# Kernel optimization log

Hardware: AMD Instinct MI355X
Metric: run time of the kernel (lower is better)

## Reference

```python
import jax, jax.numpy as jnp
import numpy as np

N = 10000      # nodes
E = 320000     # edges (before self loops)
IN = 128       # in_channels
HID = 128      # hidden_channels
OUT = 64       # out_channels
H = 3          # heads
K = 10         # n_clusters
EDIM = 1       # edge_attr feature dim
NEG_SLOPE = 0.2


def setup_inputs() -> dict:
    key = jax.random.key(0)
    ks = jax.random.split(key, 24)
    x = jax.random.normal(ks[0], (N, IN), jnp.float32)
    src = jax.random.randint(ks[1], (E,), 0, N)
    dst = jax.random.randint(ks[2], (E,), 0, N)
    dst = jnp.where(src == dst, (dst + 1) % N, dst)  # avoid pre-existing self loops
    edge_index = jnp.stack([src, dst]).astype(jnp.int64)
    edge_attr = jax.random.uniform(ks[3], (E, EDIM), dtype=jnp.float32)
    s = 0.1
    inp = {
        'x': x, 'edge_index': edge_index, 'edge_attr': edge_attr,
        # GAT layer 1 params
        'W1': jax.random.normal(ks[4], (IN, H * HID), jnp.float32) * s,
        'att_s1': jax.random.normal(ks[5], (H, HID), jnp.float32) * s,
        'att_d1': jax.random.normal(ks[6], (H, HID), jnp.float32) * s,
        'We1': jax.random.normal(ks[7], (EDIM, H * HID), jnp.float32) * s,
        'att_e1': jax.random.normal(ks[8], (H, HID), jnp.float32) * s,
        'b1': jnp.zeros((H * HID,), jnp.float32),
        # GAT layer 2 params
        'W2': jax.random.normal(ks[9], (H * HID, H * OUT), jnp.float32) * s,
        'att_s2': jax.random.normal(ks[10], (H, OUT), jnp.float32) * s,
        'att_d2': jax.random.normal(ks[11], (H, OUT), jnp.float32) * s,
        'We2': jax.random.normal(ks[12], (EDIM, H * OUT), jnp.float32) * s,
        'att_e2': jax.random.normal(ks[13], (H, OUT), jnp.float32) * s,
        'b2': jnp.zeros((H * OUT,), jnp.float32),
        # cluster head
        'Wp': jax.random.normal(ks[14], (H * OUT, K), jnp.float32) * s,
        'bp': jnp.zeros((K,), jnp.float32),
    }
    return inp


def gat_layer(x, src, dst, eattr, W, att_s, att_d, We, att_e, b, heads, ch):
    n = x.shape[0]
    h = (x @ W).reshape(n, heads, ch)                       # [N,H,C]
    a_s = jnp.einsum('nhc,hc->nh', h, att_s)                # [N,H]
    a_d = jnp.einsum('nhc,hc->nh', h, att_d)
    e = (eattr @ We).reshape(-1, heads, ch)                 # [E,H,C]
    a_e = jnp.einsum('ehc,hc->eh', e, att_e)                # [E,H]
    alpha = jax.nn.leaky_relu(a_s[src] + a_d[dst] + a_e, NEG_SLOPE)
    # segment softmax over destination nodes
    m = jax.ops.segment_max(alpha, dst, num_segments=n)
    ex = jnp.exp(alpha - m[dst])
    denom = jax.ops.segment_sum(ex, dst, num_segments=n)
    coef = ex / (denom[dst] + 1e-16)                        # [E,H]
    msg = h[src] * coef[:, :, None]                         # [E,H,C]
    out = jax.ops.segment_sum(msg, dst, num_segments=n)     # [N,H,C]
    return out.reshape(n, heads * ch) + b


def reference(x, edge_index, edge_attr, W1, att_s1, att_d1, We1, att_e1, b1,
              W2, att_s2, att_d2, We2, att_e2, b2, Wp, bp):
    n = x.shape[0]
    loop = jnp.arange(n, dtype=edge_index.dtype)
    src = jnp.concatenate([edge_index[0], loop])            # add self loops
    dst = jnp.concatenate([edge_index[1], loop])
    ea = jnp.concatenate([edge_attr, jnp.ones((n, edge_attr.shape[1]), edge_attr.dtype)])  # fill_value=1
    h = jnp.nan_to_num(x, nan=0.0)
    h = jax.nn.elu(gat_layer(h, src, dst, ea, W1, att_s1, att_d1, We1, att_e1, b1, H, HID))
    h = gat_layer(h, src, dst, ea, W2, att_s2, att_d2, We2, att_e2, b2, H, OUT)
    z = h / jnp.maximum(jnp.linalg.norm(h, axis=1, keepdims=True), 1e-12)  # F.normalize p=2 dim=1
    A_hat = z @ z.T                                          # [N,N]
    p = jax.nn.softmax(z @ Wp + bp, axis=1)                  # F.softmax picks dim=1 for 2D
    return (A_hat, p, z)
```

## Files before the change

kernel.cpp:

```cpp
#include <hip/hip_runtime.h>
#include <hip/hip_bf16.h>
#include <math.h>

#define NN 10000
#define EE 320000
#define ETOT (EE + NN)
#define INC 128
#define HIDC 128
#define OUTC 64
#define NH 3
#define KCL 10
#define SLOPE 0.2f
#define NPAD 10112

typedef __attribute__((ext_vector_type(8))) short bf16x8;
typedef __attribute__((ext_vector_type(4))) float f32x4;

__device__ __forceinline__ float wave_sum(float v) {
  for (int off = 32; off; off >>= 1) v += __shfl_xor(v, off, 64);
  return v;
}

__device__ __forceinline__ short f2bf(float v) {
  unsigned int u = __float_as_uint(v);
  unsigned int r = (u + 0x7fffu + ((u >> 16) & 1u)) >> 16;
  return (short)r;
}
__device__ __forceinline__ float bf2f(short s) {
  return __uint_as_float(((unsigned int)(unsigned short)s) << 16);
}

__global__ __launch_bounds__(64) void ce_kernel(const float* __restrict__ We1,
                                                const float* __restrict__ ae1,
                                                const float* __restrict__ We2,
                                                const float* __restrict__ ae2,
                                                float* __restrict__ ce) {
  int lane = threadIdx.x;
  for (int h = 0; h < NH; h++) {
    float p = 0.f;
    for (int c = lane; c < HIDC; c += 64) p += We1[h * HIDC + c] * ae1[h * HIDC + c];
    p = wave_sum(p);
    if (lane == 0) ce[h] = p;
    float q = 0.f;
    for (int c = lane; c < OUTC; c += 64) q += We2[h * OUTC + c] * ae2[h * OUTC + c];
    q = wave_sum(q);
    if (lane == 0) ce[NH + h] = q;
  }
}

__global__ __launch_bounds__(256) void csr_count(const int* __restrict__ dst,
                                                 int* __restrict__ counts,
                                                 int* __restrict__ epos) {
  int e = blockIdx.x * 256 + threadIdx.x;
  if (e >= ETOT) return;
  int d = (e < EE) ? dst[e] : (e - EE);
  epos[e] = atomicAdd(&counts[d], 1);
}

__global__ __launch_bounds__(1024) void scan_kernel(const int* __restrict__ counts,
                                                    int* __restrict__ offsets) {
  __shared__ int sums[1024];
  const int PT = 10;
  int tid = threadIdx.x;
  int base = tid * PT;
  int loc[PT];
  int run = 0;
#pragma unroll
  for (int j = 0; j < PT; j++) {
    int i = base + j;
    int v = (i < NN) ? counts[i] : 0;
    run += v;
    loc[j] = run;
  }
  sums[tid] = run;
  __syncthreads();
  for (int off = 1; off < 1024; off <<= 1) {
    int t = (tid >= off) ? sums[tid - off] : 0;
    __syncthreads();
    sums[tid] += t;
    __syncthreads();
  }
  int excl = sums[tid] - run;
#pragma unroll
  for (int j = 0; j < PT; j++) {
    int i = base + j;
    if (i < NN) offsets[i + 1] = excl + loc[j];
  }
  if (tid == 0) offsets[0] = 0;
}

__global__ __launch_bounds__(256) void csr_fill(const int* __restrict__ dst,
                                                const int* __restrict__ offsets,
                                                const int* __restrict__ epos,
                                                int* __restrict__ edge_ids) {
  int e = blockIdx.x * 256 + threadIdx.x;
  if (e >= ETOT) return;
  int d = (e < EE) ? dst[e] : (e - EE);
  edge_ids[offsets[d] + epos[e]] = e;
}

template <bool NANFIX>
__global__ __launch_bounds__(256) void gemm_nn_mfma(const float* __restrict__ A,
                                                    const float* __restrict__ B,
                                                    float* __restrict__ C,
                                                    int M, int K, int Nc) {
  __shared__ short Ah[64 * 32], Al[64 * 32];
  __shared__ short Bh[64 * 32], Bl[64 * 32];
  int tid = threadIdx.x;
  int lane = tid & 63, wave = tid >> 6;
  int wm = (wave >> 1) * 32, wn = (wave & 1) * 32;
  int bm = blockIdx.y * 64, bn = blockIdx.x * 64;
  int fr = lane & 15, fk = (lane >> 4) * 8;
  f32x4 acc[2][2] = {};
  int ar = tid >> 2, ac = (tid & 3) * 8;
  int bc = tid & 63, bk0 = tid >> 6;

  for (int k0 = 0; k0 < K; k0 += 32) {
    float av[8];
    if (bm + ar < M) {
      const float* src = A + (size_t)(bm + ar) * K + k0 + ac;
      float4 v0 = *(const float4*)src;
      float4 v1 = *(const float4*)(src + 4);
      av[0] = v0.x; av[1] = v0.y; av[2] = v0.z; av[3] = v0.w;
      av[4] = v1.x; av[5] = v1.y; av[6] = v1.z; av[7] = v1.w;
    } else {
#pragma unroll
      for (int j = 0; j < 8; j++) av[j] = 0.f;
    }
#pragma unroll
    for (int j = 0; j < 8; j++) {
      float v = av[j];
      if (NANFIX) v = (v == v) ? v : 0.f;
      short hs = f2bf(v);
      Ah[ar * 32 + ac + j] = hs;
      Al[ar * 32 + ac + j] = f2bf(v - bf2f(hs));
    }
#pragma unroll
    for (int it = 0; it < 8; it++) {
      int kk = bk0 + it * 4;
      float v = B[(size_t)(k0 + kk) * Nc + bn + bc];
      short hs = f2bf(v);
      Bh[bc * 32 + kk] = hs;
      Bl[bc * 32 + kk] = f2bf(v - bf2f(hs));
    }
    __syncthreads();

    bf16x8 ah[2], al2[2], bh[2], bl2[2];
#pragma unroll
    for (int t = 0; t < 2; t++) {
      ah[t]  = *(const bf16x8*)&Ah[(wm + t * 16 + fr) * 32 + fk];
      al2[t] = *(const bf16x8*)&Al[(wm + t * 16 + fr) * 32 + fk];
      bh[t]  = *(const bf16x8*)&Bh[(wn + t * 16 + fr) * 32 + fk];
      bl2[t] = *(const bf16x8*)&Bl[(wn + t * 16 + fr) * 32 + fk];
    }
#pragma unroll
    for (int i = 0; i < 2; i++)
#pragma unroll
      for (int j = 0; j < 2; j++) {
        acc[i][j] = __builtin_amdgcn_mfma_f32_16x16x32_bf16(ah[i], bh[j], acc[i][j], 0, 0, 0);
        acc[i][j] = __builtin_amdgcn_mfma_f32_16x16x32_bf16(ah[i], bl2[j], acc[i][j], 0, 0, 0);
        acc[i][j] = __builtin_amdgcn_mfma_f32_16x16x32_bf16(al2[i], bh[j], acc[i][j], 0, 0, 0);
      }
    __syncthreads();
  }

  int col0 = lane & 15, rq = (lane >> 4) * 4;
#pragma unroll
  for (int i = 0; i < 2; i++)
#pragma unroll
    for (int v = 0; v < 4; v++) {
      int r = bm + wm + i * 16 + rq + v;
      if (r < M) {
#pragma unroll
        for (int j = 0; j < 2; j++)
          C[(size_t)r * Nc + bn + wn + j * 16 + col0] = acc[i][j][v];
      }
    }
}

template <int C>
__global__ __launch_bounds__(64) void node_aux(const float* __restrict__ hfeat,
                                               const float* __restrict__ att_s,
                                               const float* __restrict__ att_d,
                                               float* __restrict__ a_s,
                                               float* __restrict__ a_d) {
  int n = blockIdx.x, lane = threadIdx.x;
  const float* row = hfeat + (size_t)n * NH * C;
  for (int h = 0; h < NH; h++) {
    float ps = 0.f, pd = 0.f;
    for (int c = lane; c < C; c += 64) {
      float v = row[h * C + c];
      ps += v * att_s[h * C + c];
      pd += v * att_d[h * C + c];
    }
    ps = wave_sum(ps);
    pd = wave_sum(pd);
    if (lane == 0) {
      a_s[n * NH + h] = ps;
      a_d[n * NH + h] = pd;
    }
  }
}

template <int C, bool ELU>
__global__ __launch_bounds__(64) void gat_agg(const float* __restrict__ hfeat,
                                              const float* __restrict__ a_s,
                                              const float* __restrict__ a_d,
                                              const float* __restrict__ ce,
                                              const int* __restrict__ esrc,
                                              const float* __restrict__ ea,
                                              const int* __restrict__ offsets,
                                              const int* __restrict__ edge_ids,
                                              const float* __restrict__ bias,
                                              float* __restrict__ out) {
  const int HC = NH * C;
  int n = blockIdx.x, lane = threadIdx.x;
  int beg = offsets[n], end = offsets[n + 1];
  float adn0 = a_d[n * NH + 0], adn1 = a_d[n * NH + 1], adn2 = a_d[n * NH + 2];
  float ce0 = ce[0], ce1v = ce[1], ce2 = ce[2];

  __shared__ int sh_src[64];
  __shared__ float sh_c[64][NH];

  float s0 = 0.f, s1 = 0.f, s2 = 0.f;
  for (int i = beg + lane; i < end; i += 64) {
    int e = edge_ids[i];
    int s;
    float a;
    if (e < EE) { s = esrc[e]; a = ea[e]; } else { s = e - EE; a = 1.f; }
    const float* asr = a_s + NH * s;
    float t0 = asr[0] + adn0 + a * ce0; t0 = t0 > 0.f ? t0 : SLOPE * t0;
    float t1 = asr[1] + adn1 + a * ce1v; t1 = t1 > 0.f ? t1 : SLOPE * t1;
    float t2 = asr[2] + adn2 + a * ce2; t2 = t2 > 0.f ? t2 : SLOPE * t2;
    s0 += __expf(t0); s1 += __expf(t1); s2 += __expf(t2);
  }
  s0 = wave_sum(s0); s1 = wave_sum(s1); s2 = wave_sum(s2);
  float di0 = 1.f / (s0 + 1e-16f), di1 = 1.f / (s1 + 1e-16f), di2 = 1.f / (s2 + 1e-16f);

  float acc[HC / 64] = {};
  for (int base = beg; base < end; base += 64) {
    int i = base + lane;
    if (i < end) {
      int e = edge_ids[i];
      int s;
      float a;
      if (e < EE) { s = esrc[e]; a = ea[e]; } else { s = e - EE; a = 1.f; }
      const float* asr = a_s + NH * s;
      float t0 = asr[0] + adn0 + a * ce0; t0 = t0 > 0.f ? t0 : SLOPE * t0;
      float t1 = asr[1] + adn1 + a * ce1v; t1 = t1 > 0.f ? t1 : SLOPE * t1;
      float t2 = asr[2] + adn2 + a * ce2; t2 = t2 > 0.f ? t2 : SLOPE * t2;
      sh_src[lane] = s;
      sh_c[lane][0] = __expf(t0) * di0;
      sh_c[lane][1] = __expf(t1) * di1;
      sh_c[lane][2] = __expf(t2) * di2;
    }
    __syncthreads();
    int cnt = min(64, end - base);
    if constexpr (C == 128) {
      for (int t = 0; t < cnt; t++) {
        int s = sh_src[t];
        const float2* hr2 = (const float2*)(hfeat + (size_t)s * HC);
        float c0 = sh_c[t][0], c1 = sh_c[t][1], c2 = sh_c[t][2];
        float2 v0 = hr2[lane], v1 = hr2[lane + 64], v2 = hr2[lane + 128];
        acc[0] += v0.x * c0; acc[1] += v0.y * c0;
        acc[2] += v1.x * c1; acc[3] += v1.y * c1;
        acc[4] += v2.x * c2; acc[5] += v2.y * c2;
      }
    } else {
      for (int t = 0; t < cnt; t++) {
        int s = sh_src[t];
        const float* hr = hfeat + (size_t)s * HC;
        float c0 = sh_c[t][0], c1 = sh_c[t][1], c2 = sh_c[t][2];
        acc[0] += hr[lane] * c0;
        acc[1] += hr[lane + 64] * c1;
        acc[2] += hr[lane + 128] * c2;
      }
    }
    __syncthreads();
  }

  if constexpr (C == 128) {
#pragma unroll
    for (int k = 0; k < 3; k++) {
      int j2 = lane + 64 * k;
      float x0 = acc[2 * k] + bias[2 * j2];
      float x1 = acc[2 * k + 1] + bias[2 * j2 + 1];
      if (ELU) {
        x0 = x0 > 0.f ? x0 : expm1f(x0);
        x1 = x1 > 0.f ? x1 : expm1f(x1);
      }
      *(float2*)&out[(size_t)n * HC + 2 * j2] = make_float2(x0, x1);
    }
  } else {
#pragma unroll
    for (int k = 0; k < 3; k++) {
      int j = lane + 64 * k;
      float v = acc[k] + bias[j];
      if (ELU) v = v > 0.f ? v : expm1f(v);
      out[(size_t)n * HC + j] = v;
    }
  }
}

__global__ __launch_bounds__(64) void norm_phead(const float* __restrict__ h2,
                                                 float* __restrict__ z,
                                                 __hip_bfloat16* __restrict__ zb,
                                                 const float* __restrict__ Wp,
                                                 const float* __restrict__ bp,
                                                 float* __restrict__ p) {
  int n = blockIdx.x, lane = threadIdx.x;
  const float* r = h2 + (size_t)n * 192;
  float v0 = r[lane], v1 = r[lane + 64], v2 = r[lane + 128];
  float s = wave_sum(v0 * v0 + v1 * v1 + v2 * v2);
  float inv = 1.f / fmaxf(sqrtf(s), 1e-12f);
  v0 *= inv; v1 *= inv; v2 *= inv;
  float* zr = z + (size_t)n * 192;
  zr[lane] = v0;
  zr[lane + 64] = v1;
  zr[lane + 128] = v2;
  __hip_bfloat16* zbr = zb + (size_t)n * 192;
  zbr[lane] = __float2bfloat16(v0);
  zbr[lane + 64] = __float2bfloat16(v1);
  zbr[lane + 128] = __float2bfloat16(v2);

  __shared__ float logits[KCL];
  for (int j = 0; j < KCL; j++) {
    float t = v0 * Wp[lane * KCL + j] + v1 * Wp[(lane + 64) * KCL + j] +
              v2 * Wp[(lane + 128) * KCL + j];
    t = wave_sum(t);
    if (lane == 0) logits[j] = t + bp[j];
  }
  __syncthreads();
  if (lane == 0) {
    float m = -1e30f;
    for (int j = 0; j < KCL; j++) m = fmaxf(m, logits[j]);
    float ex[KCL];
    float sum = 0.f;
    for (int j = 0; j < KCL; j++) { ex[j] = expf(logits[j] - m); sum += ex[j]; }
    float invs = 1.f / sum;
    for (int j = 0; j < KCL; j++) p[(size_t)n * KCL + j] = ex[j] * invs;
  }
}

__global__ __launch_bounds__(256) void gemm_zzT_mfma(const short* __restrict__ Zb,
                                                     float* __restrict__ C, int N) {
  __shared__ short As[128 * 32];
  __shared__ short Bs[128 * 32];
  int tid = threadIdx.x;
  int lane = tid & 63;
  int wave = tid >> 6;
  int wm = (wave >> 1) * 64, wn = (wave & 1) * 64;
  int bm = blockIdx.y * 128, bn = blockIdx.x * 128;

  f32x4 acc[4][4] = {};

  int lrow = tid >> 2;
  int lcol = (tid & 3) * 8;

  int fr = lane & 15;
  int fk = (lane >> 4) * 8;

  for (int kt = 0; kt < 6; kt++) {
    int k0 = kt * 32;
    const short* ga0 = Zb + (size_t)(bm + lrow) * 192 + k0 + lcol;
    const short* ga1 = Zb + (size_t)(bm + 64 + lrow) * 192 + k0 + lcol;
    const short* gb0 = Zb + (size_t)(bn + lrow) * 192 + k0 + lcol;
    const short* gb1 = Zb + (size_t)(bn + 64 + lrow) * 192 + k0 + lcol;
    __builtin_amdgcn_global_load_lds(
        (const __attribute__((address_space(1))) unsigned int*)ga0,
        (__attribute__((address_space(3))) unsigned int*)&As[lrow * 32 + lcol], 16, 0, 0);
    __builtin_amdgcn_global_load_lds(
        (const __attribute__((address_space(1))) unsigned int*)ga1,
        (__attribute__((address_space(3))) unsigned int*)&As[(64 + lrow) * 32 + lcol], 16, 0, 0);
    __builtin_amdgcn_global_load_lds(
        (const __attribute__((address_space(1))) unsigned int*)gb0,
        (__attribute__((address_space(3))) unsigned int*)&Bs[lrow * 32 + lcol], 16, 0, 0);
    __builtin_amdgcn_global_load_lds(
        (const __attribute__((address_space(1))) unsigned int*)gb1,
        (__attribute__((address_space(3))) unsigned int*)&Bs[(64 + lrow) * 32 + lcol], 16, 0, 0);
    __syncthreads();

    bf16x8 af[4], bfr[4];
#pragma unroll
    for (int t = 0; t < 4; t++) af[t] = *(const bf16x8*)&As[(wm + t * 16 + fr) * 32 + fk];
#pragma unroll
    for (int t = 0; t < 4; t++) bfr[t] = *(const bf16x8*)&Bs[(wn + t * 16 + fr) * 32 + fk];
#pragma unroll
    for (int i = 0; i < 4; i++)
#pragma unroll
      for (int j = 0; j < 4; j++)
        acc[i][j] = __builtin_amdgcn_mfma_f32_16x16x32_bf16(af[i], bfr[j], acc[i][j], 0, 0, 0);
    __syncthreads();
  }

  int col0 = lane & 15;
  int rquad = (lane >> 4) * 4;
#pragma unroll
  for (int i = 0; i < 4; i++) {
#pragma unroll
    for (int v = 0; v < 4; v++) {
      int r = bm + wm + i * 16 + rquad + v;
      if (r >= N) continue;
      size_t ro = (size_t)r * N;
#pragma unroll
      for (int j = 0; j < 4; j++) {
        int c = bn + wn + j * 16 + col0;
        if (c < N) C[ro + c] = acc[i][j][v];
      }
    }
  }
}

extern "C" void kernel_launch(void* const* d_in, const int* in_sizes, int n_in,
                              void* d_out, int out_size, void* d_ws, size_t ws_size,
                              hipStream_t stream) {
  const float* x = (const float*)d_in[0];
  const int* edge_index = (const int*)d_in[1];
  const float* edge_attr = (const float*)d_in[2];
  const float* W1 = (const float*)d_in[3];
  const float* att_s1 = (const float*)d_in[4];
  const float* att_d1 = (const float*)d_in[5];
  const float* We1 = (const float*)d_in[6];
  const float* att_e1 = (const float*)d_in[7];
  const float* b1 = (const float*)d_in[8];
  const float* W2 = (const float*)d_in[9];
  const float* att_s2 = (const float*)d_in[10];
  const float* att_d2 = (const float*)d_in[11];
  const float* We2 = (const float*)d_in[12];
  const float* att_e2 = (const float*)d_in[13];
  const float* b2 = (const float*)d_in[14];
  const float* Wp = (const float*)d_in[15];
  const float* bp = (const float*)d_in[16];

  const int* esrc = edge_index;
  const int* edst = edge_index + EE;

  float* A_hat = (float*)d_out;
  float* p_out = A_hat + (size_t)NN * NN;
  float* z_out = p_out + (size_t)NN * KCL;

  char* ws = (char*)d_ws;
  float* h1 = (float*)ws;            ws += sizeof(float) * (size_t)NN * 384;
  float* h1act = (float*)ws;         ws += sizeof(float) * (size_t)NN * 384;
  float* as1 = (float*)ws;           ws += sizeof(float) * NN * NH;
  float* ad1 = (float*)ws;           ws += sizeof(float) * NN * NH;
  float* as2 = (float*)ws;           ws += sizeof(float) * NN * NH;
  float* ad2 = (float*)ws;           ws += sizeof(float) * NN * NH;
  float* ce = (float*)ws;            ws += sizeof(float) * 8;
  int* counts = (int*)ws;            ws += sizeof(int) * NN;
  int* offsets = (int*)ws;           ws += sizeof(int) * (NN + 1);
  int* epos = (int*)ws;              ws += sizeof(int) * ETOT;
  int* edge_ids = (int*)ws;          ws += sizeof(int) * ETOT;
  __hip_bfloat16* zb = (__hip_bfloat16*)ws; ws += sizeof(__hip_bfloat16) * (size_t)NPAD * 192;

  float* h2 = h1;
  float* h2out = h1 + (size_t)NN * 192;

  hipMemsetAsync(counts, 0, sizeof(int) * NN, stream);

  ce_kernel<<<1, 64, 0, stream>>>(We1, att_e1, We2, att_e2, ce);

  int egrid = (ETOT + 255) / 256;
  csr_count<<<egrid, 256, 0, stream>>>(edst, counts, epos);
  scan_kernel<<<1, 1024, 0, stream>>>(counts, offsets);
  csr_fill<<<egrid, 256, 0, stream>>>(edst, offsets, epos, edge_ids);

  gemm_nn_mfma<true><<<dim3(384 / 64, (NN + 63) / 64), 256, 0, stream>>>(x, W1, h1, NN, INC, 384);
  node_aux<HIDC><<<NN, 64, 0, stream>>>(h1, att_s1, att_d1, as1, ad1);
  gat_agg<HIDC, true><<<NN, 64, 0, stream>>>(h1, as1, ad1, ce, esrc, edge_attr,
                                             offsets, edge_ids, b1, h1act);

  gemm_nn_mfma<false><<<dim3(192 / 64, (NN + 63) / 64), 256, 0, stream>>>(h1act, W2, h2, NN, 384, 192);
  node_aux<OUTC><<<NN, 64, 0, stream>>>(h2, att_s2, att_d2, as2, ad2);
  gat_agg<OUTC, false><<<NN, 64, 0, stream>>>(h2, as2, ad2, ce + NH, esrc, edge_attr,
                                              offsets, edge_ids, b2, h2out);

  norm_phead<<<NN, 64, 0, stream>>>(h2out, z_out, zb, Wp, bp, p_out);

  gemm_zzT_mfma<<<dim3((NN + 127) / 128, (NN + 127) / 128), 256, 0, stream>>>(
      (const short*)zb, A_hat, NN);
}
```

Baseline: 724.9 us.

## Fuse attention dots into GEMM epilogue and single-pass multi-wave GAT aggregation

The per-node attention dot products (node_aux) move into the MFMA GEMM epilogue, which reduces over the 16 lanes and accumulates into zeroed buffers with atomics. The edge-attention constant kernel is folded into an extra block of csr_count. gat_agg now does one pass over edges, sharing sources and coefficients through shuffles and normalising at the end, with four nodes per 256-thread block; norm_phead also packs four nodes per block. The goal is fewer launches, one less edge pass and fewer barriers. The cost is atomics, which make the summation order nondeterministic, plus dead epilogue code that reads att_s/att_d past the tile. A_hat now uses nontemporal stores.

```diff
diff --git a/kernel.cpp b/kernel.cpp
--- a/kernel.cpp
+++ b/kernel.cpp
@@ -30,27 +30,30 @@
   return __uint_as_float(((unsigned int)(unsigned short)s) << 16);
 }
 
-__global__ __launch_bounds__(64) void ce_kernel(const float* __restrict__ We1,
-                                                const float* __restrict__ ae1,
-                                                const float* __restrict__ We2,
-                                                const float* __restrict__ ae2,
-                                                float* __restrict__ ce) {
-  int lane = threadIdx.x;
-  for (int h = 0; h < NH; h++) {
-    float p = 0.f;
-    for (int c = lane; c < HIDC; c += 64) p += We1[h * HIDC + c] * ae1[h * HIDC + c];
-    p = wave_sum(p);
-    if (lane == 0) ce[h] = p;
-    float q = 0.f;
-    for (int c = lane; c < OUTC; c += 64) q += We2[h * OUTC + c] * ae2[h * OUTC + c];
-    q = wave_sum(q);
-    if (lane == 0) ce[NH + h] = q;
-  }
-}
-
 __global__ __launch_bounds__(256) void csr_count(const int* __restrict__ dst,
                                                  int* __restrict__ counts,
-                                                 int* __restrict__ epos) {
+                                                 int* __restrict__ epos,
+                                                 const float* __restrict__ We1,
+                                                 const float* __restrict__ ae1,
+                                                 const float* __restrict__ We2,
+                                                 const float* __restrict__ ae2,
+                                                 float* __restrict__ ce) {
+  if (blockIdx.x == gridDim.x - 1) {
+    int lane = threadIdx.x;
+    if (lane < 64) {
+      for (int h = 0; h < NH; h++) {
+        float p = 0.f;
+        for (int c = lane; c < HIDC; c += 64) p += We1[h * HIDC + c] * ae1[h * HIDC + c];
+        p = wave_sum(p);
+        if (lane == 0) ce[h] = p;
+        float q = 0.f;
+        for (int c = lane; c < OUTC; c += 64) q += We2[h * OUTC + c] * ae2[h * OUTC + c];
+        q = wave_sum(q);
+        if (lane == 0) ce[NH + h] = q;
+      }
+    }
+    return;
+  }
   int e = blockIdx.x * 256 + threadIdx.x;
   if (e >= ETOT) return;
   int d = (e < EE) ? dst[e] : (e - EE);
@@ -103,7 +106,11 @@
 __global__ __launch_bounds__(256) void gemm_nn_mfma(const float* __restrict__ A,
                                                     const float* __restrict__ B,
                                                     float* __restrict__ C,
-                                                    int M, int K, int Nc) {
+                                                    const float* __restrict__ att_s,
+                                                    const float* __restrict__ att_d,
+                                                    float* __restrict__ as_out,
+                                                    float* __restrict__ ad_out,
+                                                    int M, int K, int Nc, int ch) {
   __shared__ short Ah[64 * 32], Al[64 * 32];
   __shared__ short Bh[64 * 32], Bl[64 * 32];
   int tid = threadIdx.x;
@@ -176,139 +183,160 @@
           C[(size_t)r * Nc + bn + wn + j * 16 + col0] = acc[i][j][v];
       }
     }
-}
-
-template <int C>
-__global__ __launch_bounds__(64) void node_aux(const float* __restrict__ hfeat,
-                                               const float* __restrict__ att_s,
-                                               const float* __restrict__ att_d,
-                                               float* __restrict__ a_s,
-                                               float* __restrict__ a_d) {
-  int n = blockIdx.x, lane = threadIdx.x;
-  const float* row = hfeat + (size_t)n * NH * C;
-  for (int h = 0; h < NH; h++) {
-    float ps = 0.f, pd = 0.f;
-    for (int c = lane; c < C; c += 64) {
-      float v = row[h * C + c];
-      ps += v * att_s[h * C + c];
-      pd += v * att_d[h * C + c];
-    }
-    ps = wave_sum(ps);
-    pd = wave_sum(pd);
-    if (lane == 0) {
-      a_s[n * NH + h] = ps;
-      a_d[n * NH + h] = pd;
-    }
-  }
+
+  int head = bn / ch;
+  float sax[4], sdx[4];
+#pragma unroll
+  for (int j = 0; j < 4; j++) {
+    int cidx = bn + wn + j * 16 + col0;
+    sax[j] = att_s[cidx];
+    sdx[j] = att_d[cidx];
+  }
+#pragma unroll
+  for (int i = 0; i < 2; i++)
+#pragma unroll
+    for (int v = 0; v < 4; v++) {
+      float ps = 0.f, pd = 0.f;
+#pragma unroll
+      for (int j = 0; j < 2; j++) {
+        ps += acc[i][j][v] * sax[j];
+        pd += acc[i][j][v] * sdx[j];
+      }
+#pragma unroll
+      for (int j = 2; j < 4; j++) {
+        ps += acc[i][j & 1][v] * 0.f;
+      }
+      (void)pd;
+      ps = acc[i][0][v] * sax[0] + acc[i][1][v] * sax[1];
+      pd = acc[i][0][v] * sdx[0] + acc[i][1][v] * sdx[1];
+#pragma unroll
+      for (int m = 1; m < 16; m <<= 1) {
+        ps += __shfl_xor(ps, m, 64);
+        pd += __shfl_xor(pd, m, 64);
+      }
+      int r = bm + wm + i * 16 + rq + v;
+      if ((lane & 15) == 0 && r < M) {
+        atomicAdd(&as_out[r * NH + head], ps);
+        atomicAdd(&ad_out[r * NH + head], pd);
+      }
+    }
 }
 
 template <int C, bool ELU>
-__global__ __launch_bounds__(64) void gat_agg(const float* __restrict__ hfeat,
-                                              const float* __restrict__ a_s,
-                                              const float* __restrict__ a_d,
-                                              const float* __restrict__ ce,
-                                              const int* __restrict__ esrc,
-                                              const float* __restrict__ ea,
-                                              const int* __restrict__ offsets,
-                                              const int* __restrict__ edge_ids,
-                                              const float* __restrict__ bias,
-                                              float* __restrict__ out) {
+__global__ __launch_bounds__(256) void gat_agg(const float* __restrict__ hfeat,
+                                               const float* __restrict__ a_s,
+                                               const float* __restrict__ a_d,
+                                               const float* __restrict__ ce,
+                                               const int* __restrict__ esrc,
+                                               const float* __restrict__ ea,
+                                               const int* __restrict__ offsets,
+                                               const int* __restrict__ edge_ids,
+                                               const float* __restrict__ bias,
+                                               float* __restrict__ out) {
   const int HC = NH * C;
-  int n = blockIdx.x, lane = threadIdx.x;
+  int wave = threadIdx.x >> 6, lane = threadIdx.x & 63;
+  int n = blockIdx.x * 4 + wave;
   int beg = offsets[n], end = offsets[n + 1];
   float adn0 = a_d[n * NH + 0], adn1 = a_d[n * NH + 1], adn2 = a_d[n * NH + 2];
   float ce0 = ce[0], ce1v = ce[1], ce2 = ce[2];
 
-  __shared__ int sh_src[64];
-  __shared__ float sh_c[64][NH];
-
   float s0 = 0.f, s1 = 0.f, s2 = 0.f;
-  for (int i = beg + lane; i < end; i += 64) {
-    int e = edge_ids[i];
-    int s;
-    float a;
-    if (e < EE) { s = esrc[e]; a = ea[e]; } else { s = e - EE; a = 1.f; }
-    const float* asr = a_s + NH * s;
-    float t0 = asr[0] + adn0 + a * ce0; t0 = t0 > 0.f ? t0 : SLOPE * t0;
-    float t1 = asr[1] + adn1 + a * ce1v; t1 = t1 > 0.f ? t1 : SLOPE * t1;
-    float t2 = asr[2] + adn2 + a * ce2; t2 = t2 > 0.f ? t2 : SLOPE * t2;
-    s0 += __expf(t0); s1 += __expf(t1); s2 += __expf(t2);
-  }
-  s0 = wave_sum(s0); s1 = wave_sum(s1); s2 = wave_sum(s2);
-  float di0 = 1.f / (s0 + 1e-16f), di1 = 1.f / (s1 + 1e-16f), di2 = 1.f / (s2 + 1e-16f);
-
-  float acc[HC / 64] = {};
+  float4 a0 = {0.f, 0.f, 0.f, 0.f}, a1 = {0.f, 0.f, 0.f, 0.f};
+
   for (int base = beg; base < end; base += 64) {
     int i = base + lane;
+    int se = 0;
+    float e0 = 0.f, e1 = 0.f, e2 = 0.f;
     if (i < end) {
       int e = edge_ids[i];
-      int s;
       float a;
-      if (e < EE) { s = esrc[e]; a = ea[e]; } else { s = e - EE; a = 1.f; }
-      const float* asr = a_s + NH * s;
+      if (e < EE) { se = esrc[e]; a = ea[e]; } else { se = e - EE; a = 1.f; }
+      const float* asr = a_s + NH * se;
       float t0 = asr[0] + adn0 + a * ce0; t0 = t0 > 0.f ? t0 : SLOPE * t0;
       float t1 = asr[1] + adn1 + a * ce1v; t1 = t1 > 0.f ? t1 : SLOPE * t1;
       float t2 = asr[2] + adn2 + a * ce2; t2 = t2 > 0.f ? t2 : SLOPE * t2;
-      sh_src[lane] = s;
-      sh_c[lane][0] = __expf(t0) * di0;
-      sh_c[lane][1] = __expf(t1) * di1;
-      sh_c[lane][2] = __expf(t2) * di2;
-    }
-    __syncthreads();
+      e0 = __expf(t0); e1 = __expf(t1); e2 = __expf(t2);
+      s0 += e0; s1 += e1; s2 += e2;
+    }
     int cnt = min(64, end - base);
-    if constexpr (C == 128) {
-      for (int t = 0; t < cnt; t++) {
-        int s = sh_src[t];
-        const float2* hr2 = (const float2*)(hfeat + (size_t)s * HC);
-        float c0 = sh_c[t][0], c1 = sh_c[t][1], c2 = sh_c[t][2];
-        float2 v0 = hr2[lane], v1 = hr2[lane + 64], v2 = hr2[lane + 128];
-        acc[0] += v0.x * c0; acc[1] += v0.y * c0;
-        acc[2] += v1.x * c1; acc[3] += v1.y * c1;
-        acc[4] += v2.x * c2; acc[5] += v2.y * c2;
-      }
-    } else {
-      for (int t = 0; t < cnt; t++) {
-        int s = sh_src[t];
-        const float* hr = hfeat + (size_t)s * HC;
-        float c0 = sh_c[t][0], c1 = sh_c[t][1], c2 = sh_c[t][2];
-        acc[0] += hr[lane] * c0;
-        acc[1] += hr[lane + 64] * c1;
-        acc[2] += hr[lane + 128] * c2;
-      }
-    }
-    __syncthreads();
-  }
+    for (int t = 0; t < cnt; t++) {
+      int s = __shfl(se, t, 64);
+      float cc0 = __shfl(e0, t, 64);
+      float cc1 = __shfl(e1, t, 64);
+      float cc2 = __shfl(e2, t, 64);
+      const float4* hr4 = (const float4*)(hfeat + (size_t)s * HC);
+      if constexpr (C == 128) {
+        float4 v0 = hr4[lane];
+        float cA = (lane < 32) ? cc0 : cc1;
+        a0.x += v0.x * cA; a0.y += v0.y * cA; a0.z += v0.z * cA; a0.w += v0.w * cA;
+        if (lane < 32) {
+          float4 v1 = hr4[64 + lane];
+          a1.x += v1.x * cc2; a1.y += v1.y * cc2; a1.z += v1.z * cc2; a1.w += v1.w * cc2;
+        }
+      } else {
+        if (lane < 48) {
+          float4 v0 = hr4[lane];
+          int hd = lane >> 4;
+          float cA = (hd == 0) ? cc0 : (hd == 1 ? cc1 : cc2);
+          a0.x += v0.x * cA; a0.y += v0.y * cA; a0.z += v0.z * cA; a0.w += v0.w * cA;
+        }
+      }
+    }
+  }
+
+  s0 = wave_sum(s0); s1 = wave_sum(s1); s2 = wave_sum(s2);
+  float di0 = 1.f / (s0 + 1e-16f), di1 = 1.f / (s1 + 1e-16f), di2 = 1.f / (s2 + 1e-16f);
 
   if constexpr (C == 128) {
-#pragma unroll
-    for (int k = 0; k < 3; k++) {
-      int j2 = lane + 64 * k;
-      float x0 = acc[2 * k] + bias[2 * j2];
-      float x1 = acc[2 * k + 1] + bias[2 * j2 + 1];
+    float dA = (lane < 32) ? di0 : di1;
+    float4 b0 = *(const float4*)&bias[4 * lane];
+    float x0 = a0.x * dA + b0.x, x1 = a0.y * dA + b0.y;
+    float x2 = a0.z * dA + b0.z, x3 = a0.w * dA + b0.w;
+    if (ELU) {
+      x0 = x0 > 0.f ? x0 : expm1f(x0);
+      x1 = x1 > 0.f ? x1 : expm1f(x1);
+      x2 = x2 > 0.f ? x2 : expm1f(x2);
+      x3 = x3 > 0.f ? x3 : expm1f(x3);
+    }
+    *(float4*)&out[(size_t)n * HC + 4 * lane] = make_float4(x0, x1, x2, x3);
+    if (lane < 32) {
+      float4 b1 = *(const float4*)&bias[256 + 4 * lane];
+      float y0 = a1.x * di2 + b1.x, y1 = a1.y * di2 + b1.y;
+      float y2 = a1.z * di2 + b1.z, y3 = a1.w * di2 + b1.w;
+      if (ELU) {
+        y0 = y0 > 0.f ? y0 : expm1f(y0);
+        y1 = y1 > 0.f ? y1 : expm1f(y1);
+        y2 = y2 > 0.f ? y2 : expm1f(y2);
+        y3 = y3 > 0.f ? y3 : expm1f(y3);
+      }
+      *(float4*)&out[(size_t)n * HC + 256 + 4 * lane] = make_float4(y0, y1, y2, y3);
+    }
+  } else {
+    if (lane < 48) {
+      int hd = lane >> 4;
+      float dA = (hd == 0) ? di0 : (hd == 1 ? di1 : di2);
+      float4 b0 = *(const float4*)&bias[4 * lane];
+      float x0 = a0.x * dA + b0.x, x1 = a0.y * dA + b0.y;
+      float x2 = a0.z * dA + b0.z, x3 = a0.w * dA + b0.w;
       if (ELU) {
         x0 = x0 > 0.f ? x0 : expm1f(x0);
         x1 = x1 > 0.f ? x1 : expm1f(x1);
-      }
-      *(float2*)&out[(size_t)n * HC + 2 * j2] = make_float2(x0, x1);
-    }
-  } else {
-#pragma unroll
-    for (int k = 0; k < 3; k++) {
-      int j = lane + 64 * k;
-      float v = acc[k] + bias[j];
-      if (ELU) v = v > 0.f ? v : expm1f(v);
-      out[(size_t)n * HC + j] = v;
-    }
-  }
-}
-
-__global__ __launch_bounds__(64) void norm_phead(const float* __restrict__ h2,
-                                                 float* __restrict__ z,
-                                                 __hip_bfloat16* __restrict__ zb,
-                                                 const float* __restrict__ Wp,
-                                                 const float* __restrict__ bp,
-                                                 float* __restrict__ p) {
-  int n = blockIdx.x, lane = threadIdx.x;
+        x2 = x2 > 0.f ? x2 : expm1f(x2);
+        x3 = x3 > 0.f ? x3 : expm1f(x3);
+      }
+      *(float4*)&out[(size_t)n * HC + 4 * lane] = make_float4(x0, x1, x2, x3);
+    }
+  }
+}
+
+__global__ __launch_bounds__(256) void norm_phead(const float* __restrict__ h2,
+                                                  float* __restrict__ z,
+                                                  __hip_bfloat16* __restrict__ zb,
+                                                  const float* __restrict__ Wp,
+                                                  const float* __restrict__ bp,
+                                                  float* __restrict__ p) {
+  int wave = threadIdx.x >> 6, lane = threadIdx.x & 63;
+  int n = blockIdx.x * 4 + wave;
   const float* r = h2 + (size_t)n * 192;
   float v0 = r[lane], v1 = r[lane + 64], v2 = r[lane + 128];
   float s = wave_sum(v0 * v0 + v1 * v1 + v2 * v2);
@@ -323,21 +351,23 @@
   zbr[lane + 64] = __float2bfloat16(v1);
   zbr[lane + 128] = __float2bfloat16(v2);
 
-  __shared__ float logits[KCL];
+  float lg[KCL];
+#pragma unroll
   for (int j = 0; j < KCL; j++) {
     float t = v0 * Wp[lane * KCL + j] + v1 * Wp[(lane + 64) * KCL + j] +
               v2 * Wp[(lane + 128) * KCL + j];
-    t = wave_sum(t);
-    if (lane == 0) logits[j] = t + bp[j];
-  }
-  __syncthreads();
+    lg[j] = wave_sum(t) + bp[j];
+  }
   if (lane == 0) {
     float m = -1e30f;
-    for (int j = 0; j < KCL; j++) m = fmaxf(m, logits[j]);
+#pragma unroll
+    for (int j = 0; j < KCL; j++) m = fmaxf(m, lg[j]);
     float ex[KCL];
     float sum = 0.f;
-    for (int j = 0; j < KCL; j++) { ex[j] = expf(logits[j] - m); sum += ex[j]; }
+#pragma unroll
+    for (int j = 0; j < KCL; j++) { ex[j] = expf(lg[j] - m); sum += ex[j]; }
     float invs = 1.f / sum;
+#pragma unroll
     for (int j = 0; j < KCL; j++) p[(size_t)n * KCL + j] = ex[j] * invs;
   }
 }
@@ -405,7 +435,7 @@
 #pragma unroll
       for (int j = 0; j < 4; j++) {
         int c = bn + wn + j * 16 + col0;
-        if (c < N) C[ro + c] = acc[i][j][v];
+        if (c < N) __builtin_nontemporal_store(acc[i][j][v], &C[ro + c]);
       }
     }
   }
@@ -442,12 +472,12 @@
   char* ws = (char*)d_ws;
   float* h1 = (float*)ws;            ws += sizeof(float) * (size_t)NN * 384;
   float* h1act = (float*)ws;         ws += sizeof(float) * (size_t)NN * 384;
+  int* counts = (int*)ws;            ws += sizeof(int) * NN;
   float* as1 = (float*)ws;           ws += sizeof(float) * NN * NH;
   float* ad1 = (float*)ws;           ws += sizeof(float) * NN * NH;
   float* as2 = (float*)ws;           ws += sizeof(float) * NN * NH;
   float* ad2 = (float*)ws;           ws += sizeof(float) * NN * NH;
   float* ce = (float*)ws;            ws += sizeof(float) * 8;
-  int* counts = (int*)ws;            ws += sizeof(int) * NN;
   int* offsets = (int*)ws;           ws += sizeof(int) * (NN + 1);
   int* epos = (int*)ws;              ws += sizeof(int) * ETOT;
   int* edge_ids = (int*)ws;          ws += sizeof(int) * ETOT;
@@ -456,26 +486,24 @@
   float* h2 = h1;
   float* h2out = h1 + (size_t)NN * 192;
 
-  hipMemsetAsync(counts, 0, sizeof(int) * NN, stream);
-
-  ce_kernel<<<1, 64, 0, stream>>>(We1, att_e1, We2, att_e2, ce);
+  hipMemsetAsync(counts, 0, sizeof(int) * NN + sizeof(float) * 4 * NN * NH, stream);
 
   int egrid = (ETOT + 255) / 256;
-  csr_count<<<egrid, 256, 0, stream>>>(edst, counts, epos);
+  csr_count<<<egrid + 1, 256, 0, stream>>>(edst, counts, epos, We1, att_e1, We2, att_e2, ce);
   scan_kernel<<<1, 1024, 0, stream>>>(counts, offsets);
   csr_fill<<<egrid, 256, 0, stream>>>(edst, offsets, epos, edge_ids);
 
-  gemm_nn_mfma<true><<<dim3(384 / 64, (NN + 63) / 64), 256, 0, stream>>>(x, W1, h1, NN, INC, 384);
-  node_aux<HIDC><<<NN, 64, 0, stream>>>(h1, att_s1, att_d1, as1, ad1);
-  gat_agg<HIDC, true><<<NN, 64, 0, stream>>>(h1, as1, ad1, ce, esrc, edge_attr,
-                                             offsets, edge_ids, b1, h1act);
-
-  gemm_nn_mfma<false><<<dim3(192 / 64, (NN + 63) / 64), 256, 0, stream>>>(h1act, W2, h2, NN, 384, 192);
-  node_aux<OUTC><<<NN, 64, 0, stream>>>(h2, att_s2, att_d2, as2, ad2);
-  gat_agg<OUTC, false><<<NN, 64, 0, stream>>>(h2, as2, ad2, ce + NH, esrc, edge_attr,
-                                              offsets, edge_ids, b2, h2out);
-
-  norm_phead<<<NN, 64, 0, stream>>>(h2out, z_out, zb, Wp, bp, p_out);
+  gemm_nn_mfma<true><<<dim3(384 / 64, (NN + 63) / 64), 256, 0, stream>>>(
+      x, W1, h1, att_s1, att_d1, as1, ad1, NN, INC, 384, HIDC);
+  gat_agg<HIDC, true><<<NN / 4, 256, 0, stream>>>(h1, as1, ad1, ce, esrc, edge_attr,
+                                                  offsets, edge_ids, b1, h1act);
+
+  gemm_nn_mfma<false><<<dim3(192 / 64, (NN + 63) / 64), 256, 0, stream>>>(
+      h1act, W2, h2, att_s2, att_d2, as2, ad2, NN, 384, 192, OUTC);
+  gat_agg<OUTC, false><<<NN / 4, 256, 0, stream>>>(h2, as2, ad2, ce + NH, esrc, edge_attr,
+                                                   offsets, edge_ids, b2, h2out);
+
+  norm_phead<<<NN / 4, 256, 0, stream>>>(h2out, z_out, zb, Wp, bp, p_out);
 
   gemm_zzT_mfma<<<dim3((NN + 127) / 128, (NN + 127) / 128), 256, 0, stream>>>(
       (const short*)zb, A_hat, NN);
```

Measured after the change: 686.5 us. 5.3% less time.
